# Performance work log

Measured on AMD Instinct MI355X. Metric: run time of the kernel, lower is better.

The kernel has to match this reference:

```python
import jax, jax.numpy as jnp
import numpy as np

M_POS = 0.5
M_NEG_SIM = 0.1
LAM_NEG = 1.0


def setup_inputs() -> dict:
    key = jax.random.key(0)
    N, d, G = 8192, 1024, 64
    codebook = jax.random.normal(key, (N, d), dtype=jnp.float32)
    base = (jnp.arange(N) // G) * G  # contiguous groups of size G (vq_to_range)
    starts = base.astype(jnp.int32)
    ends = (base + G - 1).astype(jnp.int32)
    return {"codebook": codebook, "starts": starts, "ends": ends, "max_i": N - 1}


def reference(codebook, starts, ends, max_i):
    N, d = codebook.shape
    M = min(N, int(max_i) + 1)  # rows processed by the python loop

    # cosine similarity rows [0:M] vs all N
    zn = codebook / jnp.linalg.norm(codebook, axis=-1, keepdims=True)
    cos = jnp.einsum('md,nd->mn', zn[:M], zn)  # (M, N)

    # pairwise Euclidean distances rows [0:M] vs all N via ||a-b||^2 = |a|^2+|b|^2-2ab
    sq = jnp.sum(codebook * codebook, axis=-1)  # (N,)
    dot = jnp.einsum('md,nd->mn', codebook[:M], codebook)  # (M, N)
    d2 = jnp.maximum(sq[:M, None] + sq[None, :] - 2.0 * dot, 0.0)

    j = jnp.arange(N)[None, :]
    i = jnp.arange(M)[:, None]
    in_range = (j >= starts[:M, None]) & (j <= ends[:M, None])
    pos_mask = in_range & (j != i)
    # original: group_mask[i]=False then neg = ~group_mask, so i is in negatives
    neg_mask = (~in_range) | (j == i)

    pos_cnt = jnp.sum(pos_mask, axis=-1)
    neg_cnt = jnp.sum(neg_mask, axis=-1)

    # safe sqrt: only evaluate on positive-mask entries
    D = jnp.sqrt(jnp.where(pos_mask, d2, 1.0))
    pos_term = jnp.square(jax.nn.relu(D - M_POS)) * pos_mask
    pos_pull = jnp.sum(pos_term, axis=-1) / jnp.maximum(pos_cnt, 1)

    neg_cos = jnp.clip(cos, -1.0, 1.0)
    neg_term = jnp.square(jax.nn.relu(jnp.abs(neg_cos) - M_NEG_SIM)) * neg_mask
    ortho = jnp.sum(neg_term, axis=-1) / jnp.maximum(neg_cnt, 1)

    valid = (pos_cnt > 0) & (neg_cnt > 0)
    per_row = jnp.where(valid, pos_pull + LAM_NEG * ortho, 0.0)
    cnt = jnp.sum(valid)
    total = jnp.sum(per_row)
    return jnp.where(cnt > 0, total / jnp.maximum(cnt, 1).astype(total.dtype), jnp.zeros((), total.dtype))
```

## Files before the change

### kernel.cpp

```cpp
#include <hip/hip_runtime.h>
#include <hip/hip_bf16.h>
#include <stdint.h>

#define M_POS 0.5f
#define M_NEG 0.1f
#define LAM_NEG 1.0f

typedef __attribute__((ext_vector_type(4))) float floatx4;
typedef __attribute__((ext_vector_type(8))) int   intx8;

union Frag8 { intx8 v; int4 q[2]; };

__global__ __launch_bounds__(256) void prep_kernel(
    const float* __restrict__ cb, unsigned char* __restrict__ cb_q,
    float* __restrict__ sq, float* __restrict__ inv_norm,
    unsigned* __restrict__ zero_base, int zero_len,
    int N, int d)
{
    const int gi = blockIdx.x * 256 + threadIdx.x;
    if (gi < zero_len) zero_base[gi] = 0u;

    const int row = blockIdx.x;
    const float* src = cb + (size_t)row * d;
    unsigned char* dst = cb_q + (size_t)row * d;
    const int t = threadIdx.x;

    float s = 0.f;
    for (int c = t * 4; c < d; c += 1024) {
        float4 v = *(const float4*)(src + c);
        s += v.x * v.x + v.y * v.y + v.z * v.z + v.w * v.w;
        int pk = __builtin_amdgcn_cvt_pk_fp8_f32(v.x, v.y, 0, false);
        pk     = __builtin_amdgcn_cvt_pk_fp8_f32(v.z, v.w, pk, true);
        *(int*)(dst + c) = pk;
    }
    for (int o = 32; o > 0; o >>= 1) s += __shfl_down(s, o, 64);
    __shared__ float wsum[4];
    if ((t & 63) == 0) wsum[t >> 6] = s;
    __syncthreads();
    if (t == 0) {
        float tot = wsum[0] + wsum[1] + wsum[2] + wsum[3];
        sq[row] = tot;
        inv_norm[row] = rsqrtf(tot);
    }
}

__global__ __launch_bounds__(256, 4) void gram_loss_kernel(
    const unsigned char* __restrict__ A,
    const float* __restrict__ sq, const float* __restrict__ inv_norm,
    const int* __restrict__ starts, const int* __restrict__ ends,
    const int* __restrict__ max_ip,
    float* __restrict__ pos_acc, float* __restrict__ neg_acc,
    unsigned* __restrict__ counter, float* __restrict__ out,
    int N, int d)
{
    const int M = min(N, max_ip[0] + 1);

    const int t = blockIdx.x;
    int bx = (int)((sqrtf(8.f * (float)t + 1.f) - 1.f) * 0.5f);
    while ((bx + 1) * (bx + 2) / 2 <= t) bx++;
    while (bx * (bx + 1) / 2 > t) bx--;
    const int by = t - bx * (bx + 1) / 2;

    const int rowBase = by * 128;
    const int colBase = bx * 128;
    const bool isDiag = (by == bx);

    __shared__ alignas(16) unsigned char ldsA[128 * 128];
    __shared__ alignas(16) unsigned char ldsB[128 * 128];

    const int tid  = threadIdx.x;
    const int wave = tid >> 6;
    const int lane = tid & 63;
    const int wr = (wave >> 1) * 64;
    const int wc = (wave & 1) * 64;

    const int rl = lane & 15;
    const int g  = lane >> 4;
    const int q  = g;
    const int jlo = colBase + wc;
    const int ilo = rowBase + wr;

    int   jn[4];
    float jinv[4];
    bool  jvalid[4];
#pragma unroll
    for (int ct = 0; ct < 4; ++ct) {
        const int j = jlo + ct * 16 + rl;
        jn[ct]  = j;
        jinv[ct] = inv_norm[j];
        jvalid[ct] = (j < M);
    }
    bool posLane = false;
    {
        const int ri = ilo + lane;
        if (ri < M) posLane |= (ends[ri] >= jlo) && (starts[ri] <= jlo + 63);
        if (!isDiag) {
            const int cj = jlo + lane;
            if (cj < M) posLane |= (ends[cj] >= ilo) && (starts[cj] <= ilo + 63);
        }
    }
    const bool fullPath = (__ballot(posLane) != 0ULL);

    floatx4 acc[4][4];
#pragma unroll
    for (int a = 0; a < 4; ++a)
#pragma unroll
        for (int b = 0; b < 4; ++b) acc[a][b] = (floatx4){0.f, 0.f, 0.f, 0.f};

    const int sRow = lane >> 3;
    const int sChk = lane & 7;
    const int srcOffC = ((sChk ^ sRow) * 16);
    const int kTiles = d / 128;

    const int rx = rl & 7;
    const int c0 = (((2 * g)     ^ rx) * 16);
    const int c1 = (((2 * g + 1) ^ rx) * 16);

    for (int kt = 0; kt < kTiles; ++kt) {
        __syncthreads();
        const int k0 = kt * 128;
#pragma unroll
        for (int h = 0; h < 4; ++h) {
            const int r = wave * 32 + h * 8 + sRow;
            const unsigned char* ga = A + (size_t)(rowBase + r) * d + k0 + srcOffC;
            const unsigned char* gb = A + (size_t)(colBase + r) * d + k0 + srcOffC;
            __builtin_amdgcn_global_load_lds(
                (const __attribute__((address_space(1))) void*)ga,
                (__attribute__((address_space(3))) void*)(ldsA + r * 128 + sChk * 16), 16, 0, 0);
            __builtin_amdgcn_global_load_lds(
                (const __attribute__((address_space(1))) void*)gb,
                (__attribute__((address_space(3))) void*)(ldsB + r * 128 + sChk * 16), 16, 0, 0);
        }
        __syncthreads();

        Frag8 af[4], bf[4];
#pragma unroll
        for (int t4 = 0; t4 < 4; ++t4) {
            const unsigned char* pa = ldsA + (wr + t4 * 16 + rl) * 128;
            af[t4].q[0] = *(const int4*)(pa + c0);
            af[t4].q[1] = *(const int4*)(pa + c1);
            const unsigned char* pb = ldsB + (wc + t4 * 16 + rl) * 128;
            bf[t4].q[0] = *(const int4*)(pb + c0);
            bf[t4].q[1] = *(const int4*)(pb + c1);
        }
#pragma unroll
        for (int rt = 0; rt < 4; ++rt)
#pragma unroll
            for (int ct = 0; ct < 4; ++ct)
                acc[rt][ct] = __builtin_amdgcn_mfma_scale_f32_16x16x128_f8f6f4(
                    af[rt].v, bf[ct].v, acc[rt][ct], 0, 0, 0, 127, 0, 127);
    }

    float posc[4] = {0.f, 0.f, 0.f, 0.f};
    float negc[4] = {0.f, 0.f, 0.f, 0.f};

    if (fullPath) {
        int   jns[4], jne[4];
        float jsq[4];
#pragma unroll
        for (int ct = 0; ct < 4; ++ct) {
            jsq[ct] = sq[jn[ct]];
            jns[ct] = jvalid[ct] ? starts[jn[ct]] : 0;
            jne[ct] = jvalid[ct] ? ends[jn[ct]]   : -1;
        }
#pragma unroll
        for (int rt = 0; rt < 4; ++rt) {
            const int ibase = ilo + rt * 16 + q * 4;
#pragma unroll
            for (int reg = 0; reg < 4; ++reg) {
                const int i = ibase + reg;
                const bool rowValid = (i < M);
                const int ns = rowValid ? starts[i] : 0;
                const int ne = rowValid ? ends[i]   : -1;
                const float iinv = inv_norm[i];
                const float isq  = sq[i];
                float posp = 0.f, negp = 0.f;
#pragma unroll
                for (int ct = 0; ct < 4; ++ct) {
                    const float dot = acc[rt][ct][reg];
                    const int j = jn[ct];
                    float cosv = dot * iinv * jinv[ct];
                    cosv = fminf(fmaxf(cosv, -1.f), 1.f);
                    float tn = fmaxf(fabsf(cosv) - M_NEG, 0.f);
                    const float nterm = tn * tn;
                    const float d2 = fmaxf(isq + jsq[ct] - 2.f * dot, 0.f);
                    float tp = fmaxf(sqrtf(d2) - M_POS, 0.f);
                    const float pterm = tp * tp;
                    const bool dg = (j == i);
                    if (rowValid) {
                        const bool in_r = (j >= ns) && (j <= ne);
                        if (in_r && !dg) posp += pterm;
                        if (!in_r || dg) negp += nterm;
                    }
                    if (!isDiag && jvalid[ct]) {
                        const bool in_c = (i >= jns[ct]) && (i <= jne[ct]);
                        if (in_c && !dg) posc[ct] += pterm;
                        if (!in_c || dg) negc[ct] += nterm;
                    }
                }
#pragma unroll
                for (int m = 1; m < 16; m <<= 1) {
                    posp += __shfl_xor(posp, m, 64);
                    negp += __shfl_xor(negp, m, 64);
                }
                if (rowValid && rl == 0) {
                    atomicAdd(&pos_acc[i], posp);
                    atomicAdd(&neg_acc[i], negp);
                }
            }
        }
        if (!isDiag) {
#pragma unroll
            for (int ct = 0; ct < 4; ++ct) {
                posc[ct] += __shfl_xor(posc[ct], 16, 64);
                posc[ct] += __shfl_xor(posc[ct], 32, 64);
                negc[ct] += __shfl_xor(negc[ct], 16, 64);
                negc[ct] += __shfl_xor(negc[ct], 32, 64);
            }
            if (q == 0) {
#pragma unroll
                for (int ct = 0; ct < 4; ++ct) {
                    if (jvalid[ct]) {
                        atomicAdd(&pos_acc[jn[ct]], posc[ct]);
                        atomicAdd(&neg_acc[jn[ct]], negc[ct]);
                    }
                }
            }
        }
    } else {
#pragma unroll
        for (int rt = 0; rt < 4; ++rt) {
            const int ibase = ilo + rt * 16 + q * 4;
#pragma unroll
            for (int reg = 0; reg < 4; ++reg) {
                const int i = ibase + reg;
                const float iinv = inv_norm[i];
                float negp = 0.f;
#pragma unroll
                for (int ct = 0; ct < 4; ++ct) {
                    const float dot = acc[rt][ct][reg];
                    float cosv = dot * iinv * jinv[ct];
                    cosv = fminf(fmaxf(cosv, -1.f), 1.f);
                    float tn = fmaxf(fabsf(cosv) - M_NEG, 0.f);
                    const float nterm = tn * tn;
                    negp += nterm;
                    negc[ct] += nterm;
                }
#pragma unroll
                for (int m = 1; m < 16; m <<= 1)
                    negp += __shfl_xor(negp, m, 64);
                if ((i < M) && rl == 0)
                    atomicAdd(&neg_acc[i], negp);
            }
        }
        if (!isDiag) {
#pragma unroll
            for (int ct = 0; ct < 4; ++ct) {
                negc[ct] += __shfl_xor(negc[ct], 16, 64);
                negc[ct] += __shfl_xor(negc[ct], 32, 64);
            }
            if (q == 0) {
#pragma unroll
                for (int ct = 0; ct < 4; ++ct)
                    if (jvalid[ct])
                        atomicAdd(&neg_acc[jn[ct]], negc[ct]);
            }
        }
    }

    __shared__ bool amLast;
    __syncthreads();
    if (tid == 0) {
        __threadfence();
        unsigned old = atomicAdd(counter, 1u);
        amLast = (old == (unsigned)(gridDim.x - 1));
    }
    __syncthreads();
    if (amLast) {
        __threadfence();
        float total = 0.f;
        int cnt = 0;
        for (int i = tid; i < M; i += 256) {
            const float pa = __hip_atomic_load(&pos_acc[i], __ATOMIC_RELAXED, __HIP_MEMORY_SCOPE_AGENT);
            const float na = __hip_atomic_load(&neg_acc[i], __ATOMIC_RELAXED, __HIP_MEMORY_SCOPE_AGENT);
            const int ns = starts[i], ne = ends[i];
            const int lo = max(ns, 0), hi = min(ne, N - 1);
            const int inr = max(hi - lo + 1, 0);
            const bool dg = (i >= ns) && (i <= ne);
            const int pos_cnt = inr - (dg ? 1 : 0);
            const int neg_cnt = N - inr + (dg ? 1 : 0);
            if (pos_cnt > 0 && neg_cnt > 0) {
                total += pa / (float)max(pos_cnt, 1)
                       + LAM_NEG * na / (float)max(neg_cnt, 1);
                cnt++;
            }
        }
        for (int o = 32; o > 0; o >>= 1) {
            total += __shfl_down(total, o, 64);
            cnt   += __shfl_down(cnt, o, 64);
        }
        __shared__ float fin_ts[4];
        __shared__ int   fin_cs[4];
        if ((tid & 63) == 0) { fin_ts[tid >> 6] = total; fin_cs[tid >> 6] = cnt; }
        __syncthreads();
        if (tid == 0) {
            float T = fin_ts[0] + fin_ts[1] + fin_ts[2] + fin_ts[3];
            int   C = fin_cs[0] + fin_cs[1] + fin_cs[2] + fin_cs[3];
            out[0] = (C > 0) ? T / (float)C : 0.f;
        }
    }
}

extern "C" void kernel_launch(void* const* d_in, const int* in_sizes, int n_in,
                              void* d_out, int out_size, void* d_ws, size_t ws_size,
                              hipStream_t stream) {
    const float* cb     = (const float*)d_in[0];
    const int*   starts = (const int*)d_in[1];
    const int*   ends   = (const int*)d_in[2];
    const int*   max_ip = (const int*)d_in[3];
    float* out = (float*)d_out;

    const int N = in_sizes[1];
    const int d = in_sizes[0] / N;

    char* ws = (char*)d_ws;
    unsigned char* cb_q = (unsigned char*)ws;
    size_t off = ((size_t)N * d + 255) & ~(size_t)255;
    float* sq       = (float*)(ws + off); off += (size_t)N * 4;
    float* inv_norm = (float*)(ws + off); off += (size_t)N * 4;
    float* pos_acc  = (float*)(ws + off); off += (size_t)N * 4;
    float* neg_acc  = (float*)(ws + off); off += (size_t)N * 4;
    unsigned* counter = (unsigned*)(ws + off); off += 256;

    prep_kernel<<<N, 256, 0, stream>>>(cb, cb_q, sq, inv_norm,
                                       (unsigned*)pos_acc, 2 * N + 1, N, d);

    const int nb = N / 128;
    const int nBlocks = nb * (nb + 1) / 2;
    gram_loss_kernel<<<nBlocks, 256, 0, stream>>>(cb_q, sq, inv_norm, starts, ends,
                                                  max_ip, pos_acc, neg_acc, counter,
                                                  out, N, d);
}
```

Before: 238.6 us.

## Shrink gram tiles to 64x64 single-wave blocks without block barriers

The gram/loss kernel goes from 128x128 tiles run by four waves to 64x64 tiles run by one 64-thread wave, with about four times as many triangular blocks. Block-wide __syncthreads in the K loop is replaced by an s_waitcnt on the wave's own global-to-LDS loads, and the final reduction drops its cross-wave LDS step. The aim is to remove barrier stalls and gain scheduling flexibility. The cost is that each wave loads twice as many fp8 bytes per MFMA, since A/B tile reuse is halved, and the single LDS buffer per wave is not double-buffered.

```diff
diff --git a/kernel.cpp b/kernel.cpp
--- a/kernel.cpp
+++ b/kernel.cpp
@@ -44,7 +44,7 @@
     }
 }
 
-__global__ __launch_bounds__(256, 4) void gram_loss_kernel(
+__global__ __launch_bounds__(64) void gram_loss_kernel(
     const unsigned char* __restrict__ A,
     const float* __restrict__ sq, const float* __restrict__ inv_norm,
     const int* __restrict__ starts, const int* __restrict__ ends,
@@ -61,45 +61,14 @@
     while (bx * (bx + 1) / 2 > t) bx--;
     const int by = t - bx * (bx + 1) / 2;
 
-    const int rowBase = by * 128;
-    const int colBase = bx * 128;
+    const int rowBase = by * 64;
+    const int colBase = bx * 64;
     const bool isDiag = (by == bx);
 
-    __shared__ alignas(16) unsigned char ldsA[128 * 128];
-    __shared__ alignas(16) unsigned char ldsB[128 * 128];
-
-    const int tid  = threadIdx.x;
-    const int wave = tid >> 6;
-    const int lane = tid & 63;
-    const int wr = (wave >> 1) * 64;
-    const int wc = (wave & 1) * 64;
-
-    const int rl = lane & 15;
-    const int g  = lane >> 4;
-    const int q  = g;
-    const int jlo = colBase + wc;
-    const int ilo = rowBase + wr;
-
-    int   jn[4];
-    float jinv[4];
-    bool  jvalid[4];
-#pragma unroll
-    for (int ct = 0; ct < 4; ++ct) {
-        const int j = jlo + ct * 16 + rl;
-        jn[ct]  = j;
-        jinv[ct] = inv_norm[j];
-        jvalid[ct] = (j < M);
-    }
-    bool posLane = false;
-    {
-        const int ri = ilo + lane;
-        if (ri < M) posLane |= (ends[ri] >= jlo) && (starts[ri] <= jlo + 63);
-        if (!isDiag) {
-            const int cj = jlo + lane;
-            if (cj < M) posLane |= (ends[cj] >= ilo) && (starts[cj] <= ilo + 63);
-        }
-    }
-    const bool fullPath = (__ballot(posLane) != 0ULL);
+    __shared__ alignas(16) unsigned char ldsA[64 * 128];
+    __shared__ alignas(16) unsigned char ldsB[64 * 128];
+
+    const int lane = threadIdx.x;
 
     floatx4 acc[4][4];
 #pragma unroll
@@ -112,16 +81,17 @@
     const int srcOffC = ((sChk ^ sRow) * 16);
     const int kTiles = d / 128;
 
+    const int rl = lane & 15;
+    const int g  = lane >> 4;
     const int rx = rl & 7;
     const int c0 = (((2 * g)     ^ rx) * 16);
     const int c1 = (((2 * g + 1) ^ rx) * 16);
 
     for (int kt = 0; kt < kTiles; ++kt) {
-        __syncthreads();
         const int k0 = kt * 128;
 #pragma unroll
-        for (int h = 0; h < 4; ++h) {
-            const int r = wave * 32 + h * 8 + sRow;
+        for (int h = 0; h < 8; ++h) {
+            const int r = h * 8 + sRow;
             const unsigned char* ga = A + (size_t)(rowBase + r) * d + k0 + srcOffC;
             const unsigned char* gb = A + (size_t)(colBase + r) * d + k0 + srcOffC;
             __builtin_amdgcn_global_load_lds(
@@ -131,15 +101,15 @@
                 (const __attribute__((address_space(1))) void*)gb,
                 (__attribute__((address_space(3))) void*)(ldsB + r * 128 + sChk * 16), 16, 0, 0);
         }
-        __syncthreads();
+        __builtin_amdgcn_s_waitcnt(0x0f70);
 
         Frag8 af[4], bf[4];
 #pragma unroll
         for (int t4 = 0; t4 < 4; ++t4) {
-            const unsigned char* pa = ldsA + (wr + t4 * 16 + rl) * 128;
+            const unsigned char* pa = ldsA + (t4 * 16 + rl) * 128;
             af[t4].q[0] = *(const int4*)(pa + c0);
             af[t4].q[1] = *(const int4*)(pa + c1);
-            const unsigned char* pb = ldsB + (wc + t4 * 16 + rl) * 128;
+            const unsigned char* pb = ldsB + (t4 * 16 + rl) * 128;
             bf[t4].q[0] = *(const int4*)(pb + c0);
             bf[t4].q[1] = *(const int4*)(pb + c1);
         }
@@ -150,6 +120,32 @@
                 acc[rt][ct] = __builtin_amdgcn_mfma_scale_f32_16x16x128_f8f6f4(
                     af[rt].v, bf[ct].v, acc[rt][ct], 0, 0, 0, 127, 0, 127);
     }
+
+    const int q  = g;
+    const int jlo = colBase;
+    const int ilo = rowBase;
+
+    int   jn[4];
+    float jinv[4];
+    bool  jvalid[4];
+#pragma unroll
+    for (int ct = 0; ct < 4; ++ct) {
+        const int j = jlo + ct * 16 + rl;
+        jn[ct]  = j;
+        jinv[ct] = inv_norm[j];
+        jvalid[ct] = (j < M);
+    }
+
+    bool posLane = false;
+    {
+        const int ri = ilo + lane;
+        if (ri < M) posLane |= (ends[ri] >= jlo) && (starts[ri] <= jlo + 63);
+        if (!isDiag) {
+            const int cj = jlo + lane;
+            if (cj < M) posLane |= (ends[cj] >= ilo) && (starts[cj] <= ilo + 63);
+        }
+    }
+    const bool fullPath = (__ballot(posLane) != 0ULL);
 
     float posc[4] = {0.f, 0.f, 0.f, 0.f};
     float negc[4] = {0.f, 0.f, 0.f, 0.f};
@@ -270,7 +266,7 @@
 
     __shared__ bool amLast;
     __syncthreads();
-    if (tid == 0) {
+    if (lane == 0) {
         __threadfence();
         unsigned old = atomicAdd(counter, 1u);
         amLast = (old == (unsigned)(gridDim.x - 1));
@@ -280,7 +276,7 @@
         __threadfence();
         float total = 0.f;
         int cnt = 0;
-        for (int i = tid; i < M; i += 256) {
+        for (int i = lane; i < M; i += 64) {
             const float pa = __hip_atomic_load(&pos_acc[i], __ATOMIC_RELAXED, __HIP_MEMORY_SCOPE_AGENT);
             const float na = __hip_atomic_load(&neg_acc[i], __ATOMIC_RELAXED, __HIP_MEMORY_SCOPE_AGENT);
             const int ns = starts[i], ne = ends[i];
@@ -299,15 +295,8 @@
             total += __shfl_down(total, o, 64);
             cnt   += __shfl_down(cnt, o, 64);
         }
-        __shared__ float fin_ts[4];
-        __shared__ int   fin_cs[4];
-        if ((tid & 63) == 0) { fin_ts[tid >> 6] = total; fin_cs[tid >> 6] = cnt; }
-        __syncthreads();
-        if (tid == 0) {
-            float T = fin_ts[0] + fin_ts[1] + fin_ts[2] + fin_ts[3];
-            int   C = fin_cs[0] + fin_cs[1] + fin_cs[2] + fin_cs[3];
-            out[0] = (C > 0) ? T / (float)C : 0.f;
-        }
+        if (lane == 0)
+            out[0] = (cnt > 0) ? total / (float)cnt : 0.f;
     }
 }
 
@@ -335,9 +324,9 @@
     prep_kernel<<<N, 256, 0, stream>>>(cb, cb_q, sq, inv_norm,
                                        (unsigned*)pos_acc, 2 * N + 1, N, d);
 
-    const int nb = N / 128;
+    const int nb = N / 64;
     const int nBlocks = nb * (nb + 1) / 2;
-    gram_loss_kernel<<<nBlocks, 256, 0, stream>>>(cb_q, sq, inv_norm, starts, ends,
-                                                  max_ip, pos_acc, neg_acc, counter,
-                                                  out, N, d);
+    gram_loss_kernel<<<nBlocks, 64, 0, stream>>>(cb_q, sq, inv_norm, starts, ends,
+                                                 max_ip, pos_acc, neg_acc, counter,
+                                                 out, N, d);
 }
```

New measurement: 408.5 us. 1.71x slower.
